# Optimization experiments

Measured on AMD Instinct MI355X. Metric: run time of the kernel, lower is better.

The kernel has to match this reference:

```python
import jax, jax.numpy as jnp
import numpy as np

SIGMA = 2.0  # gaussian decay std, matches test_cfg.sigma default


def setup_inputs() -> dict:
    key = jax.random.key(0)
    k1, k2, k3 = jax.random.split(key, 3)
    N, H, W = 200, 400, 608
    masks = jax.random.uniform(k1, (N, H, W), dtype=jnp.float32)
    scores = jax.random.uniform(k2, (N,), dtype=jnp.float32)
    labels = jax.random.randint(k3, (N,), 0, 80)
    return {"masks": masks, "scores": scores, "labels": labels}


def reference(masks, scores, labels):
    # Matrix NMS (SOLOv2): sort by score, IoU via one big matmul, triu mask,
    # per-class gaussian decay, rescale scores, re-sort.
    N = masks.shape[0]
    mask_area = masks.sum((1, 2))  # (N,)

    order = jnp.argsort(-scores)  # descending sort indices
    scores_s = scores[order]
    masks_s = masks[order]
    area_s = mask_area[order]
    labels_s = labels[order]

    flat = masks_s.reshape(N, -1)              # (N, H*W)
    inter = flat @ flat.T                       # (N, N) intersection
    iou = inter / (area_s[:, None] + area_s[None, :] - inter)
    triu = jnp.triu(jnp.ones((N, N), dtype=bool), 1)
    label_match = (labels_s[:, None] == labels_s[None, :]) & triu
    decay_iou = jnp.where(label_match, iou, 0.0)  # iou.triu(1) * label_matrix

    compensate = decay_iou.max(0)               # (N,) max IoU over higher-scored same-class
    decay_matrix = jnp.exp(-SIGMA * decay_iou ** 2)
    compensate_matrix = jnp.exp(-SIGMA * compensate[:, None] ** 2)
    decay_coef = (decay_matrix / compensate_matrix).min(0)  # (N,)

    new_scores = scores_s * decay_coef
    order2 = jnp.argsort(-new_scores)
    keep_inds = order[order2]
    return (new_scores[order2], labels_s[order2], masks_s[order2], keep_inds)
```

## Files before the change

### kernel.cpp

```cpp
#include <hip/hip_runtime.h>
#include <stdint.h>

#define N_DET 200
#define HW 243200
#define NP 208
#define NT 13
#define KSTEPS 3800
#define GS 256
#define SPB 15
#define TRI_TILES 91
#define PART_STRIDE (TRI_TILES * 256)
#define LDS_STRIDE 72
#define HWV (HW / 4)
#define GATHER_VECS (N_DET * HWV)

typedef __attribute__((ext_vector_type(8))) short bf16x8v;
typedef __attribute__((ext_vector_type(4))) float f32x4;

__device__ __forceinline__ unsigned short f32_to_bf16(float f) {
    union { float f; uint32_t i; } v; v.f = f;
    uint32_t lsb = (v.i >> 16) & 1u;
    v.i += 0x7FFFu + lsb;
    return (unsigned short)(v.i >> 16);
}

__device__ __forceinline__ void pack8(const float4& a, const float4& b, uint4& out) {
    unsigned short u[8];
    u[0] = f32_to_bf16(a.x); u[1] = f32_to_bf16(a.y);
    u[2] = f32_to_bf16(a.z); u[3] = f32_to_bf16(a.w);
    u[4] = f32_to_bf16(b.x); u[5] = f32_to_bf16(b.y);
    u[6] = f32_to_bf16(b.z); u[7] = f32_to_bf16(b.w);
    out = *(const uint4*)u;
}

__global__ __launch_bounds__(832) void gram_kernel(const float* __restrict__ masks,
                                                   float* __restrict__ partial) {
    __shared__ unsigned short lds[2][NP * LDS_STRIDE];
    const int kb = blockIdx.x;
    const int s0 = kb * SPB;
    const int s1 = min(KSTEPS, s0 + SPB);

    f32x4 acc[NT];
#pragma unroll
    for (int j = 0; j < NT; ++j) acc[j] = (f32x4){0.f, 0.f, 0.f, 0.f};

    const int t = threadIdx.x;
    const int lane = t & 63, wv = t >> 6;
    const int frow = lane & 15;
    const int koff = (lane >> 4) * 8;
    const int srow = t >> 3;
    const int scol = (t & 7) * 8;

    const int r0 = srow, r1 = srow + 104;
    const float* src0 = masks + (size_t)r0 * HW + scol;
    const float* src1 = masks + (size_t)r1 * HW + scol;

    float4 f0a, f0b, f1a, f1b;

    if (s0 < s1) {
        const int k0 = s0 * 64;
        if (r0 < N_DET) { f0a = *(const float4*)(src0 + k0); f0b = *(const float4*)(src0 + k0 + 4); }
        if (r1 < N_DET) { f1a = *(const float4*)(src1 + k0); f1b = *(const float4*)(src1 + k0 + 4); }
        uint4 w0, w1;
        if (r0 < N_DET) pack8(f0a, f0b, w0);
        else { const unsigned short fl = (r0 == N_DET) ? 0x3F80 : 0; unsigned short u[8];
#pragma unroll
               for (int i = 0; i < 8; ++i) u[i] = fl; w0 = *(const uint4*)u; }
        if (r1 < N_DET) pack8(f1a, f1b, w1);
        else { const unsigned short fl = (r1 == N_DET) ? 0x3F80 : 0; unsigned short u[8];
#pragma unroll
               for (int i = 0; i < 8; ++i) u[i] = fl; w1 = *(const uint4*)u; }
        *(uint4*)&lds[0][r0 * LDS_STRIDE + scol] = w0;
        *(uint4*)&lds[0][r1 * LDS_STRIDE + scol] = w1;
        __syncthreads();

        int cur = 0;
        for (int s = s0; s < s1; ++s) {
            const bool has_next = (s + 1 < s1);
            if (has_next) {
                const int kn = (s + 1) * 64;
                if (r0 < N_DET) { f0a = *(const float4*)(src0 + kn); f0b = *(const float4*)(src0 + kn + 4); }
                if (r1 < N_DET) { f1a = *(const float4*)(src1 + kn); f1b = *(const float4*)(src1 + kn + 4); }
            }

            const unsigned short* bp = &lds[cur][0];
            bf16x8v a0 = *(const bf16x8v*)&bp[(wv * 16 + frow) * LDS_STRIDE + koff];
            bf16x8v a1 = *(const bf16x8v*)&bp[(wv * 16 + frow) * LDS_STRIDE + 32 + koff];
#pragma unroll
            for (int jt = 0; jt < NT; ++jt) {
                if (jt < wv) continue;
                bf16x8v b0, b1;
                if (jt == wv) { b0 = a0; b1 = a1; }
                else {
                    b0 = *(const bf16x8v*)&bp[(jt * 16 + frow) * LDS_STRIDE + koff];
                    b1 = *(const bf16x8v*)&bp[(jt * 16 + frow) * LDS_STRIDE + 32 + koff];
                }
                acc[jt] = __builtin_amdgcn_mfma_f32_16x16x32_bf16(a0, b0, acc[jt], 0, 0, 0);
                acc[jt] = __builtin_amdgcn_mfma_f32_16x16x32_bf16(a1, b1, acc[jt], 0, 0, 0);
            }

            if (has_next) {
                uint4 w0, w1;
                if (r0 < N_DET) pack8(f0a, f0b, w0);
                else { const unsigned short fl = (r0 == N_DET) ? 0x3F80 : 0; unsigned short u[8];
#pragma unroll
                       for (int i = 0; i < 8; ++i) u[i] = fl; w0 = *(const uint4*)u; }
                if (r1 < N_DET) pack8(f1a, f1b, w1);
                else { const unsigned short fl = (r1 == N_DET) ? 0x3F80 : 0; unsigned short u[8];
#pragma unroll
                       for (int i = 0; i < 8; ++i) u[i] = fl; w1 = *(const uint4*)u; }
                *(uint4*)&lds[cur ^ 1][r0 * LDS_STRIDE + scol] = w0;
                *(uint4*)&lds[cur ^ 1][r1 * LDS_STRIDE + scol] = w1;
            }
            __syncthreads();
            cur ^= 1;
        }
    }

    float* pp = partial + (size_t)kb * PART_STRIDE;
    const int tbase = wv * 13 - (wv * (wv - 1)) / 2 - wv;
    const int row16 = (lane >> 4) * 4;
    const int col16 = lane & 15;
#pragma unroll
    for (int jt = 0; jt < NT; ++jt) {
        if (jt < wv) continue;
        const int tile = tbase + jt;
#pragma unroll
        for (int r = 0; r < 4; ++r)
            pp[tile * 256 + (row16 + r) * 16 + col16] = acc[jt][r];
    }
}

__global__ void reduce_kernel(const float* __restrict__ partial,
                              float* __restrict__ gram) {
    const int tr = blockIdx.x, tc = blockIdx.y;
    if (tc < tr) return;
    const int tile = tr * 13 - (tr * (tr - 1)) / 2 + (tc - tr);
    const int idx = threadIdx.x;
    const float* p = partial + tile * 256 + idx;
    float s = 0.f;
#pragma unroll 32
    for (int g = 0; g < GS; ++g) s += p[(size_t)g * PART_STRIDE];
    const int r = tr * 16 + (idx >> 4);
    const int c = tc * 16 + (idx & 15);
    gram[r * NP + c] = s;
    if (tr != tc) gram[c * NP + r] = s;
}

__global__ __launch_bounds__(1024) void nms_kernel(const float* __restrict__ scores_in,
                                                   const int* __restrict__ labels,
                                                   const float* __restrict__ gram,
                                                   float* __restrict__ out_scores,
                                                   float* __restrict__ out_labels,
                                                   float* __restrict__ out_keep) {
    __shared__ float sc[N_DET];
    __shared__ int   lab[N_DET];
    __shared__ float ar[N_DET];
    __shared__ int   order_[N_DET];
    __shared__ float sc_s[N_DET];
    __shared__ int   lab_s[N_DET];
    __shared__ float ar_s[N_DET];
    __shared__ float comp[N_DET];
    __shared__ float part[N_DET][5];
    __shared__ int   ipart[N_DET][5];
    __shared__ float nsc[N_DET];
    __shared__ int   ord2[N_DET];

    const int t = threadIdx.x;
    const int i5 = t / 5, s5 = t - i5 * 5;

    if (t < N_DET) {
        sc[t]  = scores_in[t];
        lab[t] = labels[t];
        ar[t]  = gram[N_DET * NP + t];
    }
    __syncthreads();

    if (t < 1000) {
        const float si = sc[i5];
        int r = 0;
        for (int j = s5; j < N_DET; j += 5) {
            const float sj = sc[j];
            if (sj > si || (sj == si && j < i5)) ++r;
        }
        ipart[i5][s5] = r;
    }
    __syncthreads();
    if (t < N_DET) {
        const int r = ipart[t][0] + ipart[t][1] + ipart[t][2] + ipart[t][3] + ipart[t][4];
        order_[r] = t;
    }
    __syncthreads();
    if (t < N_DET) { const int o = order_[t]; sc_s[t] = sc[o]; lab_s[t] = lab[o]; ar_s[t] = ar[o]; }
    __syncthreads();

    if (t < 1000) {
        float m = 0.f;
        const int oj = order_[i5];
        const float aj = ar_s[i5];
        const int lj = lab_s[i5];
        for (int i = s5; i < i5; i += 5) {
            if (lab_s[i] == lj) {
                const float g = gram[order_[i] * NP + oj];
                const float iou = g / (ar_s[i] + aj - g);
                m = fmaxf(m, iou);
            }
        }
        part[i5][s5] = m;
    }
    __syncthreads();
    if (t < N_DET)
        comp[t] = fmaxf(fmaxf(fmaxf(part[t][0], part[t][1]), fmaxf(part[t][2], part[t][3])), part[t][4]);
    __syncthreads();

    if (t < 1000) {
        float mn = 1e30f;
        const int oj = order_[i5];
        const float aj = ar_s[i5];
        const int lj = lab_s[i5];
        for (int i = s5; i < N_DET; i += 5) {
            float d = 0.f;
            if (i < i5 && lab_s[i] == lj) {
                const float g = gram[order_[i] * NP + oj];
                d = g / (ar_s[i] + aj - g);
            }
            const float c = comp[i];
            const float val = expf(-2.0f * (d * d - c * c));
            mn = fminf(mn, val);
        }
        part[i5][s5] = mn;
    }
    __syncthreads();
    if (t < N_DET) {
        const float mn = fminf(fminf(fminf(part[t][0], part[t][1]), fminf(part[t][2], part[t][3])), part[t][4]);
        nsc[t] = sc_s[t] * mn;
    }
    __syncthreads();

    if (t < 1000) {
        const float si = nsc[i5];
        int r = 0;
        for (int k = s5; k < N_DET; k += 5) {
            const float sk = nsc[k];
            if (sk > si || (sk == si && k < i5)) ++r;
        }
        ipart[i5][s5] = r;
    }
    __syncthreads();
    if (t < N_DET) {
        const int r = ipart[t][0] + ipart[t][1] + ipart[t][2] + ipart[t][3] + ipart[t][4];
        ord2[r] = t;
    }
    __syncthreads();

    if (t < N_DET) {
        const int jj = ord2[t];
        out_scores[t] = nsc[jj];
        out_labels[t] = (float)lab_s[jj];
        out_keep[t]   = (float)order_[jj];
    }
}

__global__ void gather_kernel(const f32x4* __restrict__ masks,
                              const float* __restrict__ keep,
                              f32x4* __restrict__ out_masks) {
    const int stride = gridDim.x * blockDim.x;
    for (int i = blockIdx.x * blockDim.x + threadIdx.x; i < GATHER_VECS; i += stride) {
        const int r = i / HWV;
        const int c = i - r * HWV;
        const int src = (int)keep[r];
        const f32x4 v = masks[(size_t)src * HWV + c];
        __builtin_nontemporal_store(v, &out_masks[i]);
    }
}

extern "C" void kernel_launch(void* const* d_in, const int* in_sizes, int n_in,
                              void* d_out, int out_size, void* d_ws, size_t ws_size,
                              hipStream_t stream) {
    const float* masks  = (const float*)d_in[0];
    const float* scores = (const float*)d_in[1];
    const int*   labels = (const int*)d_in[2];
    float* out = (float*)d_out;

    float* out_scores = out;
    float* out_labels = out + N_DET;
    float* out_masks  = out + 2 * N_DET;
    float* out_keep   = out + 2 * N_DET + (size_t)N_DET * HW;

    float* partial = out_masks;
    float* gram    = out_masks + (size_t)GS * PART_STRIDE;

    gram_kernel<<<GS, 832, 0, stream>>>(masks, partial);
    reduce_kernel<<<dim3(13, 13), 256, 0, stream>>>(partial, gram);
    nms_kernel<<<1, 1024, 0, stream>>>(scores, labels, gram,
                                       out_scores, out_labels, out_keep);
    gather_kernel<<<2048, 256, 0, stream>>>((const f32x4*)masks, out_keep, (f32x4*)out_masks);
}
```

Measured before the change: 132.8 us.

## Widen K tile to 128 with single LDS buffer and balanced split

Doubles the K step per iteration from 64 to 128 and drops the double-buffered LDS for a single buffer. The register prefetch of the next slab now overlaps the MFMA loop, and each thread loads and packs 32 contiguous floats covering one row instead of 8 floats for two rows. K steps are now divided evenly across the 256 blocks instead of 15 per block. The aim is to halve the barrier count and loop overhead per unit of work and to issue wider contiguous global loads. The cost is two barriers per step with no LDS double buffering, plus more registers held by the eight prefetched float4s.

Measured after the change: 151.5 us. 1.14x slower.

```diff
diff --git a/kernel.cpp b/kernel.cpp
--- a/kernel.cpp
+++ b/kernel.cpp
@@ -5,12 +5,12 @@
 #define HW 243200
 #define NP 208
 #define NT 13
-#define KSTEPS 3800
+#define BK 128
+#define KSTEPS 1900
 #define GS 256
-#define SPB 15
 #define TRI_TILES 91
 #define PART_STRIDE (TRI_TILES * 256)
-#define LDS_STRIDE 72
+#define LDS_STRIDE 136
 #define HWV (HW / 4)
 #define GATHER_VECS (N_DET * HWV)
 
@@ -24,21 +24,21 @@
     return (unsigned short)(v.i >> 16);
 }
 
-__device__ __forceinline__ void pack8(const float4& a, const float4& b, uint4& out) {
+__device__ __forceinline__ uint4 pack8(const float4& a, const float4& b) {
     unsigned short u[8];
     u[0] = f32_to_bf16(a.x); u[1] = f32_to_bf16(a.y);
     u[2] = f32_to_bf16(a.z); u[3] = f32_to_bf16(a.w);
     u[4] = f32_to_bf16(b.x); u[5] = f32_to_bf16(b.y);
     u[6] = f32_to_bf16(b.z); u[7] = f32_to_bf16(b.w);
-    out = *(const uint4*)u;
+    return *(const uint4*)u;
 }
 
 __global__ __launch_bounds__(832) void gram_kernel(const float* __restrict__ masks,
                                                    float* __restrict__ partial) {
-    __shared__ unsigned short lds[2][NP * LDS_STRIDE];
+    __shared__ unsigned short lds[NP * LDS_STRIDE];
     const int kb = blockIdx.x;
-    const int s0 = kb * SPB;
-    const int s1 = min(KSTEPS, s0 + SPB);
+    const int s0 = (kb * KSTEPS) / GS;
+    const int s1 = ((kb + 1) * KSTEPS) / GS;
 
     f32x4 acc[NT];
 #pragma unroll
@@ -48,74 +48,52 @@
     const int lane = t & 63, wv = t >> 6;
     const int frow = lane & 15;
     const int koff = (lane >> 4) * 8;
-    const int srow = t >> 3;
-    const int scol = (t & 7) * 8;
-
-    const int r0 = srow, r1 = srow + 104;
-    const float* src0 = masks + (size_t)r0 * HW + scol;
-    const float* src1 = masks + (size_t)r1 * HW + scol;
-
-    float4 f0a, f0b, f1a, f1b;
-
-    if (s0 < s1) {
-        const int k0 = s0 * 64;
-        if (r0 < N_DET) { f0a = *(const float4*)(src0 + k0); f0b = *(const float4*)(src0 + k0 + 4); }
-        if (r1 < N_DET) { f1a = *(const float4*)(src1 + k0); f1b = *(const float4*)(src1 + k0 + 4); }
-        uint4 w0, w1;
-        if (r0 < N_DET) pack8(f0a, f0b, w0);
-        else { const unsigned short fl = (r0 == N_DET) ? 0x3F80 : 0; unsigned short u[8];
-#pragma unroll
-               for (int i = 0; i < 8; ++i) u[i] = fl; w0 = *(const uint4*)u; }
-        if (r1 < N_DET) pack8(f1a, f1b, w1);
-        else { const unsigned short fl = (r1 == N_DET) ? 0x3F80 : 0; unsigned short u[8];
-#pragma unroll
-               for (int i = 0; i < 8; ++i) u[i] = fl; w1 = *(const uint4*)u; }
-        *(uint4*)&lds[0][r0 * LDS_STRIDE + scol] = w0;
-        *(uint4*)&lds[0][r1 * LDS_STRIDE + scol] = w1;
+    const int srow = t >> 2;
+    const int scol = (t & 3) * 32;
+
+    const bool live = (srow < N_DET);
+    const float* src = masks + (size_t)srow * HW + scol;
+    unsigned short* dst = &lds[srow * LDS_STRIDE + scol];
+    const unsigned short fill = (srow == N_DET) ? 0x3F80 : 0;
+
+    float4 p0, p1, p2, p3, p4, p5, p6, p7;
+
+#define LOADSTEP(S) do { const float* q = src + (S) * BK;                        \
+        if (live) { p0 = *(const float4*)(q);      p1 = *(const float4*)(q + 4);  \
+                    p2 = *(const float4*)(q + 8);  p3 = *(const float4*)(q + 12); \
+                    p4 = *(const float4*)(q + 16); p5 = *(const float4*)(q + 20); \
+                    p6 = *(const float4*)(q + 24); p7 = *(const float4*)(q + 28); } } while (0)
+
+#define PACKWRITE() do {                                                          \
+        uint4 w0, w1, w2, w3;                                                     \
+        if (live) { w0 = pack8(p0, p1); w1 = pack8(p2, p3);                       \
+                    w2 = pack8(p4, p5); w3 = pack8(p6, p7); }                     \
+        else { unsigned short u[8];                                               \
+               _Pragma("unroll") for (int i = 0; i < 8; ++i) u[i] = fill;         \
+               w0 = w1 = w2 = w3 = *(const uint4*)u; }                            \
+        *(uint4*)(dst)      = w0; *(uint4*)(dst + 8)  = w1;                       \
+        *(uint4*)(dst + 16) = w2; *(uint4*)(dst + 24) = w3; } while (0)
+
+    LOADSTEP(s0);
+    for (int s = s0; s < s1; ++s) {
         __syncthreads();
-
-        int cur = 0;
-        for (int s = s0; s < s1; ++s) {
-            const bool has_next = (s + 1 < s1);
-            if (has_next) {
-                const int kn = (s + 1) * 64;
-                if (r0 < N_DET) { f0a = *(const float4*)(src0 + kn); f0b = *(const float4*)(src0 + kn + 4); }
-                if (r1 < N_DET) { f1a = *(const float4*)(src1 + kn); f1b = *(const float4*)(src1 + kn + 4); }
-            }
-
-            const unsigned short* bp = &lds[cur][0];
-            bf16x8v a0 = *(const bf16x8v*)&bp[(wv * 16 + frow) * LDS_STRIDE + koff];
-            bf16x8v a1 = *(const bf16x8v*)&bp[(wv * 16 + frow) * LDS_STRIDE + 32 + koff];
+        PACKWRITE();
+        if (s + 1 < s1) LOADSTEP(s + 1);
+        __syncthreads();
+#pragma unroll
+        for (int ks = 0; ks < BK; ks += 32) {
+            bf16x8v a = *(const bf16x8v*)&lds[(wv * 16 + frow) * LDS_STRIDE + ks + koff];
 #pragma unroll
             for (int jt = 0; jt < NT; ++jt) {
                 if (jt < wv) continue;
-                bf16x8v b0, b1;
-                if (jt == wv) { b0 = a0; b1 = a1; }
-                else {
-                    b0 = *(const bf16x8v*)&bp[(jt * 16 + frow) * LDS_STRIDE + koff];
-                    b1 = *(const bf16x8v*)&bp[(jt * 16 + frow) * LDS_STRIDE + 32 + koff];
-                }
-                acc[jt] = __builtin_amdgcn_mfma_f32_16x16x32_bf16(a0, b0, acc[jt], 0, 0, 0);
-                acc[jt] = __builtin_amdgcn_mfma_f32_16x16x32_bf16(a1, b1, acc[jt], 0, 0, 0);
+                bf16x8v b = (jt == wv) ? a
+                          : *(const bf16x8v*)&lds[(jt * 16 + frow) * LDS_STRIDE + ks + koff];
+                acc[jt] = __builtin_amdgcn_mfma_f32_16x16x32_bf16(a, b, acc[jt], 0, 0, 0);
             }
-
-            if (has_next) {
-                uint4 w0, w1;
-                if (r0 < N_DET) pack8(f0a, f0b, w0);
-                else { const unsigned short fl = (r0 == N_DET) ? 0x3F80 : 0; unsigned short u[8];
-#pragma unroll
-                       for (int i = 0; i < 8; ++i) u[i] = fl; w0 = *(const uint4*)u; }
-                if (r1 < N_DET) pack8(f1a, f1b, w1);
-                else { const unsigned short fl = (r1 == N_DET) ? 0x3F80 : 0; unsigned short u[8];
-#pragma unroll
-                       for (int i = 0; i < 8; ++i) u[i] = fl; w1 = *(const uint4*)u; }
-                *(uint4*)&lds[cur ^ 1][r0 * LDS_STRIDE + scol] = w0;
-                *(uint4*)&lds[cur ^ 1][r1 * LDS_STRIDE + scol] = w1;
-            }
-            __syncthreads();
-            cur ^= 1;
-        }
-    }
+        }
+    }
+#undef LOADSTEP
+#undef PACKWRITE
 
     float* pp = partial + (size_t)kb * PART_STRIDE;
     const int tbase = wv * 13 - (wv * (wv - 1)) / 2 - wv;
```
